# Kernel optimization log

Hardware: AMD Instinct MI355X
Metric: run time of the kernel (lower is better)

The kernel has to match this reference:

```python
import jax, jax.numpy as jnp
import numpy as np

HEADS = 2

def gat_layer(x, edge_index, W, att, bias):
    # x: [N, Fin], W: [H*C, Fin], att: [1, H, 2C], bias: [C]
    N = x.shape[0]
    C = bias.shape[0]
    # add self loops (source_to_target: x_j from row 0, aggregate onto row 1)
    loop = jnp.arange(N, dtype=edge_index.dtype)
    src = jnp.concatenate([edge_index[0], loop])
    dst = jnp.concatenate([edge_index[1], loop])
    h = (x @ W.T).reshape(N, HEADS, C)          # [N, H, C]
    x_j = h[src]                                 # [E, H, C]
    x_i = h[dst]                                 # [E, H, C]
    x_cat = jnp.concatenate([x_i, x_j], axis=-1) # [E, H, 2C]
    alpha = (x_cat * att).sum(-1)                # [E, H]
    alpha = jnp.where(alpha >= 0, alpha, 0.2 * alpha)  # leaky_relu(0.2)
    # NOTE: module uses a global (not per-destination) normalization
    alpha = jnp.exp(alpha - alpha.max())
    alpha = alpha / (alpha.sum(axis=0, keepdims=True) + 1e-10)
    msg = x_j * alpha[..., None]                 # [E, H, C]
    aggr = jax.ops.segment_sum(msg, dst, num_segments=N)  # [N, H, C]
    return aggr.mean(axis=1) + bias              # [N, C]

def setup_inputs() -> dict:
    key = jax.random.key(0)
    ks = jax.random.split(key, 7)
    N, Fin, C = 50000, 128, 64
    E = 800000
    x = jax.random.normal(ks[0], (N, Fin), dtype=jnp.float32)
    edge_index = jax.random.randint(ks[1], (2, E), 0, N, dtype=jnp.int64)
    W1 = jax.random.normal(ks[2], (HEADS * C, Fin), dtype=jnp.float32) * 0.05
    att1 = jax.random.normal(ks[3], (1, HEADS, 2 * C), dtype=jnp.float32) * 0.05
    b1 = jnp.zeros((C,), dtype=jnp.float32)
    W2 = jax.random.normal(ks[4], (HEADS * C, C), dtype=jnp.float32) * 0.05
    att2 = jax.random.normal(ks[5], (1, HEADS, 2 * C), dtype=jnp.float32) * 0.05
    b2 = jnp.zeros((C,), dtype=jnp.float32)
    return {"x": x, "edge_index": edge_index, "W1": W1, "att1": att1,
            "b1": b1, "W2": W2, "att2": att2, "b2": b2}

def reference(x, edge_index, W1, att1, b1, W2, att2, b2):
    h = gat_layer(x, edge_index, W1, att1, b1)
    h = jax.nn.relu(h)
    # F.dropout with training flag: treated as eval (identity) for determinism
    out = gat_layer(h, edge_index, W2, att2, b2)
    return out
```

## Files before the change

### kernel.cpp

```cpp
#include <hip/hip_runtime.h>
#include <hip/hip_bf16.h>
#include <math.h>


#define HP 8
#define HG 64
#define NHISTB (HP * HG)
#define HRANGE_MAX 6272
#define NSELF 16
#define NWGT  256

using short8 = __attribute__((ext_vector_type(8))) short;
using f32x4  = __attribute__((ext_vector_type(4))) float;

__device__ __forceinline__ unsigned f2bf(float x) {
  unsigned u = __float_as_uint(x);
  return (u + 0x7fffu + ((u >> 16) & 1u)) >> 16;
}
__device__ __forceinline__ float bflo(unsigned p) { return __uint_as_float(p << 16); }
__device__ __forceinline__ float bfhi(unsigned p) { return __uint_as_float(p & 0xffff0000u); }
__device__ __forceinline__ float lrexp(float a) {
  a = a >= 0.f ? a : 0.2f * a;
  return __expf(a);
}

__device__ __forceinline__ void block_zadd(float z0, float z1,
                                           float* __restrict__ Zp) {
  __shared__ float r0[16], r1[16];
  int lane = threadIdx.x & 63, w = threadIdx.x >> 6;
  int nw = blockDim.x >> 6;
#pragma unroll
  for (int off = 32; off; off >>= 1) {
    z0 += __shfl_down(z0, off, 64);
    z1 += __shfl_down(z1, off, 64);
  }
  if (lane == 0) { r0[w] = z0; r1[w] = z1; }
  __syncthreads();
  if (threadIdx.x == 0) {
    float s0 = 0.f, s1 = 0.f;
    for (int i = 0; i < nw; ++i) { s0 += r0[i]; s1 += r1[i]; }
    atomicAdd(&Zp[0], s0);
    atomicAdd(&Zp[1], s1);
  }
}

__global__ __launch_bounds__(256) void init_ws(
    const float* __restrict__ W1, const float* __restrict__ W2,
    unsigned short* __restrict__ wbf1, unsigned short* __restrict__ wbf2,
    float* __restrict__ Z, int* __restrict__ flags) {
  int tid = blockIdx.x * 256 + threadIdx.x;
  int stride = gridDim.x * 256;
  for (int i = tid; i < 128 * 128; i += stride)
    wbf1[i] = (unsigned short)f2bf(W1[i]);
  for (int i = tid; i < 128 * 64; i += stride)
    wbf2[i] = (unsigned short)f2bf(W2[i]);
  if (tid < 4) Z[tid] = 0.f;
  if (tid < 64) flags[tid] = -1;
}

template <int FIN, bool AB16>
__global__ __launch_bounds__(256) void gemm_mfma(
    const void* __restrict__ xin, const unsigned short* __restrict__ Wb,
    const float* __restrict__ att, unsigned* __restrict__ hq,
    float* __restrict__ si, float* __restrict__ sj,
    int N,
    const int* __restrict__ dstE, unsigned short* __restrict__ partial,
    int E, int nhistb, int hstep, int eper) {
  const int tid = threadIdx.x;

  constexpr int WB = 128 * FIN * 2;
  constexpr int SMEM = (WB > HRANGE_MAX * 4) ? WB : HRANGE_MAX * 4;
  __shared__ __align__(16) unsigned char smem[SMEM];

  if ((int)blockIdx.x < nhistb) {
    int* lhist = (int*)smem;
    const int p = blockIdx.x & (HP - 1);
    const int g = blockIdx.x >> 3;
    const int lo = p * hstep;
    for (int i = tid; i < hstep; i += 256) lhist[i] = 0;
    __syncthreads();
    const int eb = g * eper;
    const int ee = min(E, eb + eper);
    int e = eb + tid;
    for (; e + 3 * 256 < ee; e += 4 * 256) {
      int d0 = dstE[e] - lo;
      int d1 = dstE[e + 256] - lo;
      int d2 = dstE[e + 2 * 256] - lo;
      int d3 = dstE[e + 3 * 256] - lo;
      if ((unsigned)d0 < (unsigned)hstep) atomicAdd(&lhist[d0], 1);
      if ((unsigned)d1 < (unsigned)hstep) atomicAdd(&lhist[d1], 1);
      if ((unsigned)d2 < (unsigned)hstep) atomicAdd(&lhist[d2], 1);
      if ((unsigned)d3 < (unsigned)hstep) atomicAdd(&lhist[d3], 1);
    }
    for (; e < ee; e += 256) {
      int d = dstE[e] - lo;
      if ((unsigned)d < (unsigned)hstep) atomicAdd(&lhist[d], 1);
    }
    __syncthreads();
    for (int i = tid; i < hstep; i += 256) {
      int node = lo + i;
      if (node < N) partial[(size_t)g * N + node] = (unsigned short)lhist[i];
    }
    return;
  }

  constexpr int KS = FIN / 32;
  constexpr int CPR = FIN / 8;
  constexpr int NCHUNK = 128 * CPR;

  unsigned short* wlds = (unsigned short*)smem;

  const int w    = tid >> 6;
  const int lane = tid & 63;
  const int cl   = lane & 15;
  const int grp  = lane >> 4;
  const int n0   = (blockIdx.x - nhistb) * 64;

  const int arow = n0 + w * 16 + cl;
  const bool avalid = arow < N;

  short8 afrag[KS];
#pragma unroll
  for (int ks = 0; ks < KS; ++ks) {
    if constexpr (AB16) {
      short8 z = {0, 0, 0, 0, 0, 0, 0, 0};
      afrag[ks] = z;
      if (avalid) {
        const unsigned short* xb = (const unsigned short*)xin;
        afrag[ks] =
            *(const short8*)(xb + (size_t)arow * FIN + ks * 32 + grp * 8);
      }
    } else {
      float4 v0 = make_float4(0.f, 0.f, 0.f, 0.f), v1 = v0;
      if (avalid) {
        const float* xf = (const float*)xin;
        const float4* xp =
            (const float4*)(xf + (size_t)arow * FIN + ks * 32 + grp * 8);
        v0 = xp[0];
        v1 = xp[1];
      }
      union { short8 s8; unsigned u[4]; } af;
      af.u[0] = f2bf(v0.x) | (f2bf(v0.y) << 16);
      af.u[1] = f2bf(v0.z) | (f2bf(v0.w) << 16);
      af.u[2] = f2bf(v1.x) | (f2bf(v1.y) << 16);
      af.u[3] = f2bf(v1.z) | (f2bf(v1.w) << 16);
      afrag[ks] = af.s8;
    }
  }

  const uint4* Wb4 = (const uint4*)Wb;
  for (int c = tid; c < NCHUNK; c += 256) {
    int row = c / CPR;
    int cc  = c & (CPR - 1);
    *(uint4*)&wlds[row * FIN + ((cc ^ (row & (CPR - 1))) * 8)] = Wb4[c];
  }
  __syncthreads();

  f32x4 acc[8];
#pragma unroll
  for (int ct = 0; ct < 8; ++ct) acc[ct] = (f32x4){0.f, 0.f, 0.f, 0.f};

  const int swz = cl & (CPR - 1);
#pragma unroll
  for (int ks = 0; ks < KS; ++ks) {
#pragma unroll
    for (int ct = 0; ct < 8; ++ct) {
      const unsigned short* bp =
          &wlds[(ct * 16 + cl) * FIN + (((ks * 4 + grp) ^ swz) * 8)];
      short8 bfrag = *(const short8*)bp;
      acc[ct] = __builtin_amdgcn_mfma_f32_16x16x32_bf16(afrag[ks], bfrag,
                                                        acc[ct], 0, 0, 0);
    }
  }

  float ai[8], aj[8];
#pragma unroll
  for (int ct = 0; ct < 8; ++ct) {
    int hd = ct >> 2;
    int cw = (ct & 3) * 16 + cl;
    ai[ct] = att[hd * 128 + cw];
    aj[ct] = att[hd * 128 + 64 + cw];
  }

#pragma unroll
  for (int r = 0; r < 4; ++r) {
    int node = n0 + w * 16 + grp * 4 + r;
    float s0i = 0.f, s0j = 0.f, s1i = 0.f, s1j = 0.f;
    unsigned wpk[4];
#pragma unroll
    for (int ct = 0; ct < 4; ++ct) {
      float v0 = acc[ct][r];
      float v1 = acc[ct + 4][r];
      s0i += v0 * ai[ct];
      s0j += v0 * aj[ct];
      s1i += v1 * ai[ct + 4];
      s1j += v1 * aj[ct + 4];
      wpk[ct] = f2bf(v0) | (f2bf(v1) << 16);
    }
#pragma unroll
    for (int off = 8; off; off >>= 1) {
      s0i += __shfl_xor(s0i, off, 64);
      s0j += __shfl_xor(s0j, off, 64);
      s1i += __shfl_xor(s1i, off, 64);
      s1j += __shfl_xor(s1j, off, 64);
    }
    if (node < N) {
#pragma unroll
      for (int ct = 0; ct < 4; ++ct)
        hq[(size_t)node * 64 + ct * 16 + cl] = wpk[ct];
      if (cl == 0) {
        si[node * 2 + 0] = s0i;
        si[node * 2 + 1] = s1i;
        sj[node * 2 + 0] = s0j;
        sj[node * 2 + 1] = s1j;
      }
    }
  }
}

__global__ __launch_bounds__(256) void scan_full(
    unsigned short* __restrict__ partial, int* __restrict__ rowptr,
    int* __restrict__ flags, int N, int Eall, int nb) {
  __shared__ int ts[256];
  __shared__ int pre_s;
  const int b = blockIdx.x, t = threadIdx.x;
  const int base = b * 1024 + t * 4;
  int r0 = 0, r1 = 0, r2 = 0, r3 = 0;
  if (base < N) {
#pragma unroll 8
    for (int g = 0; g < HG; ++g) {
      unsigned long long* p =
          (unsigned long long*)&partial[(size_t)g * N + base];
      unsigned long long v = *p;
      *p = (unsigned long long)(unsigned short)r0 |
           ((unsigned long long)(unsigned short)r1 << 16) |
           ((unsigned long long)(unsigned short)r2 << 32) |
           ((unsigned long long)(unsigned short)r3 << 48);
      r0 += (int)(v & 0xffffu);
      r1 += (int)((v >> 16) & 0xffffu);
      r2 += (int)((v >> 32) & 0xffffu);
      r3 += (int)((v >> 48) & 0xffffu);
    }
  }
  const int tot = r0 + r1 + r2 + r3;
  ts[t] = tot;
  __syncthreads();
#pragma unroll
  for (int off = 1; off < 256; off <<= 1) {
    int x = (t >= off) ? ts[t - off] : 0;
    __syncthreads();
    ts[t] += x;
    __syncthreads();
  }
  const int run_local = ts[t] - tot;
  const int blktot = ts[255];
  if (t == 0)
    __hip_atomic_store(&flags[b], blktot, __ATOMIC_RELEASE,
                       __HIP_MEMORY_SCOPE_AGENT);
  __syncthreads();
  if (t < b) {
    int v;
    do {
      v = __hip_atomic_load(&flags[t], __ATOMIC_ACQUIRE,
                            __HIP_MEMORY_SCOPE_AGENT);
    } while (v < 0);
    ts[t] = v;
  }
  __syncthreads();
  if (t == 0) {
    int acc = 0;
    for (int i = 0; i < b; ++i) acc += ts[i];
    pre_s = acc;
  }
  __syncthreads();
  int run = pre_s + run_local;
  if (base < N) {
    rowptr[base] = run;         run += r0;
    rowptr[base + 1] = run;     run += r1;
    rowptr[base + 2] = run;     run += r2;
    rowptr[base + 3] = run;
  }
  if (b == nb - 1 && t == 255) rowptr[N] = Eall;
}

__global__ __launch_bounds__(1024) void scatter_z(
    const int* __restrict__ srcE, const int* __restrict__ dstE,
    const unsigned short* __restrict__ partial, const int* __restrict__ rowptr,
    float4* __restrict__ erec,
    const float2* __restrict__ si2, const float2* __restrict__ sj2,
    float* __restrict__ Zp, int E, int hstep, int N, int eper) {
  __shared__ __align__(16) int lcur[HRANGE_MAX];
  const int tid = threadIdx.x;
  float z0 = 0.f, z1 = 0.f;

  if ((int)blockIdx.x < NSELF) {
    for (int n = blockIdx.x * 1024 + tid; n < N; n += NSELF * 1024) {
      float2 a = si2[n], b = sj2[n];
      z0 += lrexp(a.x + b.x);
      z1 += lrexp(a.y + b.y);
    }
    block_zadd(z0, z1, Zp);
    return;
  }

  const int bid = blockIdx.x - NSELF;
  const int p = bid & (HP - 1);
  const int g = bid >> 3;
  const int lo = p * hstep;
  for (int i = tid; i < hstep; i += 1024) {
    int node = lo + i;
    lcur[i] = (node < N)
                  ? rowptr[node] + (int)partial[(size_t)g * N + node]
                  : 0;
  }
  __syncthreads();

  const int eb = g * eper;
  const int ee = min(E, eb + eper);
  int e = eb + tid;
  for (; e + 3 * 1024 < ee; e += 4 * 1024) {
    int d0 = dstE[e], d1 = dstE[e + 1024];
    int d2 = dstE[e + 2 * 1024], d3 = dstE[e + 3 * 1024];
    int s0 = srcE[e], s1 = srcE[e + 1024];
    int s2 = srcE[e + 2 * 1024], s3 = srcE[e + 3 * 1024];
    int t0 = d0 - lo, t1 = d1 - lo, t2 = d2 - lo, t3 = d3 - lo;
    if ((unsigned)t0 < (unsigned)hstep) {
      float2 siv = si2[d0], sjv = sj2[s0];
      float w0 = lrexp(siv.x + sjv.x), w1 = lrexp(siv.y + sjv.y);
      z0 += w0; z1 += w1;
      erec[atomicAdd(&lcur[t0], 1)] =
          make_float4(__int_as_float(s0), __int_as_float(d0), w0, w1);
    }
    if ((unsigned)t1 < (unsigned)hstep) {
      float2 siv = si2[d1], sjv = sj2[s1];
      float w0 = lrexp(siv.x + sjv.x), w1 = lrexp(siv.y + sjv.y);
      z0 += w0; z1 += w1;
      erec[atomicAdd(&lcur[t1], 1)] =
          make_float4(__int_as_float(s1), __int_as_float(d1), w0, w1);
    }
    if ((unsigned)t2 < (unsigned)hstep) {
      float2 siv = si2[d2], sjv = sj2[s2];
      float w0 = lrexp(siv.x + sjv.x), w1 = lrexp(siv.y + sjv.y);
      z0 += w0; z1 += w1;
      erec[atomicAdd(&lcur[t2], 1)] =
          make_float4(__int_as_float(s2), __int_as_float(d2), w0, w1);
    }
    if ((unsigned)t3 < (unsigned)hstep) {
      float2 siv = si2[d3], sjv = sj2[s3];
      float w0 = lrexp(siv.x + sjv.x), w1 = lrexp(siv.y + sjv.y);
      z0 += w0; z1 += w1;
      erec[atomicAdd(&lcur[t3], 1)] =
          make_float4(__int_as_float(s3), __int_as_float(d3), w0, w1);
    }
  }
  for (; e < ee; e += 1024) {
    int d = dstE[e];
    int dd = d - lo;
    if ((unsigned)dd < (unsigned)hstep) {
      int s = srcE[e];
      float2 siv = si2[d], sjv = sj2[s];
      float w0 = lrexp(siv.x + sjv.x), w1 = lrexp(siv.y + sjv.y);
      z0 += w0; z1 += w1;
      erec[atomicAdd(&lcur[dd], 1)] =
          make_float4(__int_as_float(s), __int_as_float(d), w0, w1);
    }
  }
  block_zadd(z0, z1, Zp);
}

__global__ __launch_bounds__(1024) void z_wgt2(
    const float2* __restrict__ si2, const float2* __restrict__ sj2,
    float* __restrict__ Zp, float4* __restrict__ erec, int E, int N) {
  const int tid = threadIdx.x;
  float z0 = 0.f, z1 = 0.f;
  if ((int)blockIdx.x < NSELF) {
    for (int n = blockIdx.x * 1024 + tid; n < N; n += NSELF * 1024) {
      float2 a = si2[n], b = sj2[n];
      z0 += lrexp(a.x + b.x);
      z1 += lrexp(a.y + b.y);
    }
  } else {
    int k = (blockIdx.x - NSELF) * 1024 + tid;
    for (; k < E; k += NWGT * 1024) {
      float4 r = erec[k];
      int s = __float_as_int(r.x);
      int d = __float_as_int(r.y);
      float2 siv = si2[d];
      float2 sjv = sj2[s];
      r.z = lrexp(siv.x + sjv.x);
      r.w = lrexp(siv.y + sjv.y);
      z0 += r.z; z1 += r.w;
      erec[k] = r;
    }
  }
  block_zadd(z0, z1, Zp);
}

__device__ __forceinline__ void edge8r(
    const float4* __restrict__ erec, int k, const unsigned* __restrict__ hq,
    int lane, float& acc0, float& acc1) {
  float4 r0 = erec[k],     r1 = erec[k + 1], r2 = erec[k + 2], r3 = erec[k + 3];
  float4 r4 = erec[k + 4], r5 = erec[k + 5], r6 = erec[k + 6], r7 = erec[k + 7];
  unsigned p0 = hq[(size_t)__float_as_int(r0.x) * 64 + lane];
  unsigned p1 = hq[(size_t)__float_as_int(r1.x) * 64 + lane];
  unsigned p2 = hq[(size_t)__float_as_int(r2.x) * 64 + lane];
  unsigned p3 = hq[(size_t)__float_as_int(r3.x) * 64 + lane];
  unsigned p4 = hq[(size_t)__float_as_int(r4.x) * 64 + lane];
  unsigned p5 = hq[(size_t)__float_as_int(r5.x) * 64 + lane];
  unsigned p6 = hq[(size_t)__float_as_int(r6.x) * 64 + lane];
  unsigned p7 = hq[(size_t)__float_as_int(r7.x) * 64 + lane];
  acc0 = fmaf(bflo(p0), r0.z, acc0);  acc1 = fmaf(bfhi(p0), r0.w, acc1);
  acc0 = fmaf(bflo(p1), r1.z, acc0);  acc1 = fmaf(bfhi(p1), r1.w, acc1);
  acc0 = fmaf(bflo(p2), r2.z, acc0);  acc1 = fmaf(bfhi(p2), r2.w, acc1);
  acc0 = fmaf(bflo(p3), r3.z, acc0);  acc1 = fmaf(bfhi(p3), r3.w, acc1);
  acc0 = fmaf(bflo(p4), r4.z, acc0);  acc1 = fmaf(bfhi(p4), r4.w, acc1);
  acc0 = fmaf(bflo(p5), r5.z, acc0);  acc1 = fmaf(bfhi(p5), r5.w, acc1);
  acc0 = fmaf(bflo(p6), r6.z, acc0);  acc1 = fmaf(bfhi(p6), r6.w, acc1);
  acc0 = fmaf(bflo(p7), r7.z, acc0);  acc1 = fmaf(bfhi(p7), r7.w, acc1);
}
__device__ __forceinline__ void edge4r(
    const float4* __restrict__ erec, int k, const unsigned* __restrict__ hq,
    int lane, float& acc0, float& acc1) {
  float4 r0 = erec[k], r1 = erec[k + 1], r2 = erec[k + 2], r3 = erec[k + 3];
  unsigned p0 = hq[(size_t)__float_as_int(r0.x) * 64 + lane];
  unsigned p1 = hq[(size_t)__float_as_int(r1.x) * 64 + lane];
  unsigned p2 = hq[(size_t)__float_as_int(r2.x) * 64 + lane];
  unsigned p3 = hq[(size_t)__float_as_int(r3.x) * 64 + lane];
  acc0 = fmaf(bflo(p0), r0.z, acc0);  acc1 = fmaf(bfhi(p0), r0.w, acc1);
  acc0 = fmaf(bflo(p1), r1.z, acc0);  acc1 = fmaf(bfhi(p1), r1.w, acc1);
  acc0 = fmaf(bflo(p2), r2.z, acc0);  acc1 = fmaf(bfhi(p2), r2.w, acc1);
  acc0 = fmaf(bflo(p3), r3.z, acc0);  acc1 = fmaf(bfhi(p3), r3.w, acc1);
}
__device__ __forceinline__ void edge1r(
    int s, float w0, float w1, const unsigned* __restrict__ hq, int lane,
    float& acc0, float& acc1) {
  unsigned p = hq[(size_t)s * 64 + lane];
  acc0 = fmaf(bflo(p), w0, acc0);
  acc1 = fmaf(bfhi(p), w1, acc1);
}

__global__ __launch_bounds__(256) void csr_aggregate(
    const int* __restrict__ rowptr, const float4* __restrict__ erec,
    const unsigned* __restrict__ hq, const float2* __restrict__ si2,
    const float2* __restrict__ sj2, const float* __restrict__ Zp,
    const float* __restrict__ bias, void* __restrict__ out,
    int N, int do_relu, int bf16_out) {
  int lane = threadIdx.x & 63;
  int wid = (blockIdx.x * blockDim.x + threadIdx.x) >> 6;
  int nw = (gridDim.x * blockDim.x) >> 6;
  float z0 = 1.f / (Zp[0] + 1e-10f);
  float z1 = 1.f / (Zp[1] + 1e-10f);
  float bv = bias[lane];
  for (int n0 = wid; n0 < N; n0 += nw) {
    int n = __builtin_amdgcn_readfirstlane(n0);
    int beg = rowptr[n], end = rowptr[n + 1];
    float2 siv = si2[n];
    float2 jv = sj2[n];
    float acc0 = 0.f, acc1 = 0.f;
    edge1r(n, lrexp(siv.x + jv.x), lrexp(siv.y + jv.y), hq, lane, acc0, acc1);
    int k = beg;
    for (; k + 8 <= end; k += 8) edge8r(erec, k, hq, lane, acc0, acc1);
    if (k + 4 <= end) { edge4r(erec, k, hq, lane, acc0, acc1); k += 4; }
    for (; k < end; ++k) {
      float4 r = erec[k];
      edge1r(__float_as_int(r.x), r.z, r.w, hq, lane, acc0, acc1);
    }
    float r = 0.5f * (acc0 * z0 + acc1 * z1) + bv;
    if (do_relu) r = fmaxf(r, 0.f);
    if (bf16_out)
      ((unsigned short*)out)[(size_t)n * 64 + lane] = (unsigned short)f2bf(r);
    else
      ((float*)out)[(size_t)n * 64 + lane] = r;
  }
}

extern "C" void kernel_launch(void* const* d_in, const int* in_sizes, int n_in,
                              void* d_out, int out_size, void* d_ws, size_t ws_size,
                              hipStream_t stream) {
  const float* x    = (const float*)d_in[0];
  const int*   ei   = (const int*)d_in[1];
  const float* W1   = (const float*)d_in[2];
  const float* att1 = (const float*)d_in[3];
  const float* b1   = (const float*)d_in[4];
  const float* W2   = (const float*)d_in[5];
  const float* att2 = (const float*)d_in[6];
  const float* b2   = (const float*)d_in[7];
  float* out = (float*)d_out;

  const int N = in_sizes[0] / 128;
  const int E = in_sizes[1] / 2;
  const int* srcE = ei;
  const int* dstE = ei + E;

  unsigned* hq = (unsigned*)d_ws;
  float* si    = (float*)(hq + (size_t)N * 64);
  float* sj    = si + (size_t)N * 2;
  float* Z     = sj + (size_t)N * 2;
  float* x2    = Z + 4;
  unsigned short* partial = (unsigned short*)x2;
  unsigned short* x2b = (unsigned short*)x2;
  int* rowptr  = (int*)(x2 + (size_t)N * 64);
  int* flags   = rowptr + (N + 1);
  uintptr_t ep = ((uintptr_t)(flags + 64) + 15) & ~(uintptr_t)15;
  float4* erec = (float4*)ep;
  unsigned short* wbf1 = (unsigned short*)(erec + E);
  unsigned short* wbf2 = wbf1 + 128 * 128;

  dim3 blk(256);
  dim3 blk1k(1024);
  int nb = (N + 1023) / 1024;
  int ntiles = (N + 63) / 64;
  int hstep = (N + HP - 1) / HP;
  int eper  = (E + HG - 1) / HG;

  init_ws<<<64, blk, 0, stream>>>(W1, W2, wbf1, wbf2, Z, flags);
  gemm_mfma<128, false><<<NHISTB + ntiles, blk, 0, stream>>>(
      x, wbf1, att1, hq, si, sj, N, dstE, partial, E, NHISTB, hstep, eper);
  scan_full<<<nb, blk, 0, stream>>>(partial, rowptr, flags, N, E, nb);
  scatter_z<<<NSELF + NHISTB, blk1k, 0, stream>>>(
      srcE, dstE, partial, rowptr, erec, (const float2*)si,
      (const float2*)sj, Z, E, hstep, N, eper);
  csr_aggregate<<<4096, blk, 0, stream>>>(rowptr, erec, hq,
                                          (const float2*)si, (const float2*)sj,
                                          Z, b1, x2b, N, 1, 1);
  gemm_mfma<64, true><<<ntiles, blk, 0, stream>>>(
      x2b, wbf2, att2, hq, si, sj, N, dstE, partial, E, 0, hstep, eper);
  z_wgt2<<<NSELF + NWGT, blk1k, 0, stream>>>(
      (const float2*)si, (const float2*)sj, Z + 2, erec, E, N);
  csr_aggregate<<<4096, blk, 0, stream>>>(rowptr, erec, hq,
                                          (const float2*)si, (const float2*)sj,
                                          Z + 2, b2, out, N, 0, 0);
}
```

Measured before the change: 238.0 us.

## Shrink edge records to 8 bytes with bf16 weights and CSR-walk layer-2 weights

The per-edge record drops from a 16-byte float4 (src, dst, w0, w1) to an 8-byte uint2 holding the source index and both attention weights packed as bf16. The layer-2 weight/Z kernel now walks the CSR row by row, one wave per destination, so the destination index no longer has to be stored and si2 is read once per row. This halves erec traffic in scatter, weight recompute and both aggregations, at the cost of bf16 precision on the attention weights. Z is still summed from the full fp32 weights.

Result: slower. 329.3 us (+38.4%).

```diff
diff --git a/kernel.cpp b/kernel.cpp
--- a/kernel.cpp
+++ b/kernel.cpp
@@ -8,7 +8,6 @@
 #define NHISTB (HP * HG)
 #define HRANGE_MAX 6272
 #define NSELF 16
-#define NWGT  256
 
 using short8 = __attribute__((ext_vector_type(8))) short;
 using f32x4  = __attribute__((ext_vector_type(4))) float;
@@ -286,7 +285,7 @@
 __global__ __launch_bounds__(1024) void scatter_z(
     const int* __restrict__ srcE, const int* __restrict__ dstE,
     const unsigned short* __restrict__ partial, const int* __restrict__ rowptr,
-    float4* __restrict__ erec,
+    uint2* __restrict__ erec,
     const float2* __restrict__ si2, const float2* __restrict__ sj2,
     float* __restrict__ Zp, int E, int hstep, int N, int eper) {
   __shared__ __align__(16) int lcur[HRANGE_MAX];
@@ -329,28 +328,28 @@
       float w0 = lrexp(siv.x + sjv.x), w1 = lrexp(siv.y + sjv.y);
       z0 += w0; z1 += w1;
       erec[atomicAdd(&lcur[t0], 1)] =
-          make_float4(__int_as_float(s0), __int_as_float(d0), w0, w1);
+          make_uint2((unsigned)s0, f2bf(w0) | (f2bf(w1) << 16));
     }
     if ((unsigned)t1 < (unsigned)hstep) {
       float2 siv = si2[d1], sjv = sj2[s1];
       float w0 = lrexp(siv.x + sjv.x), w1 = lrexp(siv.y + sjv.y);
       z0 += w0; z1 += w1;
       erec[atomicAdd(&lcur[t1], 1)] =
-          make_float4(__int_as_float(s1), __int_as_float(d1), w0, w1);
+          make_uint2((unsigned)s1, f2bf(w0) | (f2bf(w1) << 16));
     }
     if ((unsigned)t2 < (unsigned)hstep) {
       float2 siv = si2[d2], sjv = sj2[s2];
       float w0 = lrexp(siv.x + sjv.x), w1 = lrexp(siv.y + sjv.y);
       z0 += w0; z1 += w1;
       erec[atomicAdd(&lcur[t2], 1)] =
-          make_float4(__int_as_float(s2), __int_as_float(d2), w0, w1);
+          make_uint2((unsigned)s2, f2bf(w0) | (f2bf(w1) << 16));
     }
     if ((unsigned)t3 < (unsigned)hstep) {
       float2 siv = si2[d3], sjv = sj2[s3];
       float w0 = lrexp(siv.x + sjv.x), w1 = lrexp(siv.y + sjv.y);
       z0 += w0; z1 += w1;
       erec[atomicAdd(&lcur[t3], 1)] =
-          make_float4(__int_as_float(s3), __int_as_float(d3), w0, w1);
+          make_uint2((unsigned)s3, f2bf(w0) | (f2bf(w1) << 16));
     }
   }
   for (; e < ee; e += 1024) {
@@ -362,34 +361,36 @@
       float w0 = lrexp(siv.x + sjv.x), w1 = lrexp(siv.y + sjv.y);
       z0 += w0; z1 += w1;
       erec[atomicAdd(&lcur[dd], 1)] =
-          make_float4(__int_as_float(s), __int_as_float(d), w0, w1);
+          make_uint2((unsigned)s, f2bf(w0) | (f2bf(w1) << 16));
     }
   }
   block_zadd(z0, z1, Zp);
 }
 
-__global__ __launch_bounds__(1024) void z_wgt2(
+__global__ __launch_bounds__(256) void wgt2_z2(
+    const int* __restrict__ rowptr, uint2* __restrict__ erec,
     const float2* __restrict__ si2, const float2* __restrict__ sj2,
-    float* __restrict__ Zp, float4* __restrict__ erec, int E, int N) {
-  const int tid = threadIdx.x;
+    float* __restrict__ Zp, int N) {
+  int lane = threadIdx.x & 63;
+  int wid = (blockIdx.x * blockDim.x + threadIdx.x) >> 6;
+  int nw = (gridDim.x * blockDim.x) >> 6;
   float z0 = 0.f, z1 = 0.f;
-  if ((int)blockIdx.x < NSELF) {
-    for (int n = blockIdx.x * 1024 + tid; n < N; n += NSELF * 1024) {
-      float2 a = si2[n], b = sj2[n];
-      z0 += lrexp(a.x + b.x);
-      z1 += lrexp(a.y + b.y);
-    }
-  } else {
-    int k = (blockIdx.x - NSELF) * 1024 + tid;
-    for (; k < E; k += NWGT * 1024) {
-      float4 r = erec[k];
-      int s = __float_as_int(r.x);
-      int d = __float_as_int(r.y);
-      float2 siv = si2[d];
-      float2 sjv = sj2[s];
-      r.z = lrexp(siv.x + sjv.x);
-      r.w = lrexp(siv.y + sjv.y);
-      z0 += r.z; z1 += r.w;
+  for (int n0 = wid; n0 < N; n0 += nw) {
+    int n = __builtin_amdgcn_readfirstlane(n0);
+    int beg = rowptr[n], end = rowptr[n + 1];
+    float2 siv = si2[n];
+    if (lane == 0) {
+      float2 jv = sj2[n];
+      z0 += lrexp(siv.x + jv.x);
+      z1 += lrexp(siv.y + jv.y);
+    }
+    for (int k = beg + lane; k < end; k += 64) {
+      uint2 r = erec[k];
+      float2 jv = sj2[(int)r.x];
+      float w0 = lrexp(siv.x + jv.x);
+      float w1 = lrexp(siv.y + jv.y);
+      z0 += w0; z1 += w1;
+      r.y = f2bf(w0) | (f2bf(w1) << 16);
       erec[k] = r;
     }
   }
@@ -397,39 +398,39 @@
 }
 
 __device__ __forceinline__ void edge8r(
-    const float4* __restrict__ erec, int k, const unsigned* __restrict__ hq,
+    const uint2* __restrict__ erec, int k, const unsigned* __restrict__ hq,
     int lane, float& acc0, float& acc1) {
-  float4 r0 = erec[k],     r1 = erec[k + 1], r2 = erec[k + 2], r3 = erec[k + 3];
-  float4 r4 = erec[k + 4], r5 = erec[k + 5], r6 = erec[k + 6], r7 = erec[k + 7];
-  unsigned p0 = hq[(size_t)__float_as_int(r0.x) * 64 + lane];
-  unsigned p1 = hq[(size_t)__float_as_int(r1.x) * 64 + lane];
-  unsigned p2 = hq[(size_t)__float_as_int(r2.x) * 64 + lane];
-  unsigned p3 = hq[(size_t)__float_as_int(r3.x) * 64 + lane];
-  unsigned p4 = hq[(size_t)__float_as_int(r4.x) * 64 + lane];
-  unsigned p5 = hq[(size_t)__float_as_int(r5.x) * 64 + lane];
-  unsigned p6 = hq[(size_t)__float_as_int(r6.x) * 64 + lane];
-  unsigned p7 = hq[(size_t)__float_as_int(r7.x) * 64 + lane];
-  acc0 = fmaf(bflo(p0), r0.z, acc0);  acc1 = fmaf(bfhi(p0), r0.w, acc1);
-  acc0 = fmaf(bflo(p1), r1.z, acc0);  acc1 = fmaf(bfhi(p1), r1.w, acc1);
-  acc0 = fmaf(bflo(p2), r2.z, acc0);  acc1 = fmaf(bfhi(p2), r2.w, acc1);
-  acc0 = fmaf(bflo(p3), r3.z, acc0);  acc1 = fmaf(bfhi(p3), r3.w, acc1);
-  acc0 = fmaf(bflo(p4), r4.z, acc0);  acc1 = fmaf(bfhi(p4), r4.w, acc1);
-  acc0 = fmaf(bflo(p5), r5.z, acc0);  acc1 = fmaf(bfhi(p5), r5.w, acc1);
-  acc0 = fmaf(bflo(p6), r6.z, acc0);  acc1 = fmaf(bfhi(p6), r6.w, acc1);
-  acc0 = fmaf(bflo(p7), r7.z, acc0);  acc1 = fmaf(bfhi(p7), r7.w, acc1);
+  uint2 r0 = erec[k],     r1 = erec[k + 1], r2 = erec[k + 2], r3 = erec[k + 3];
+  uint2 r4 = erec[k + 4], r5 = erec[k + 5], r6 = erec[k + 6], r7 = erec[k + 7];
+  unsigned p0 = hq[(size_t)r0.x * 64 + lane];
+  unsigned p1 = hq[(size_t)r1.x * 64 + lane];
+  unsigned p2 = hq[(size_t)r2.x * 64 + lane];
+  unsigned p3 = hq[(size_t)r3.x * 64 + lane];
+  unsigned p4 = hq[(size_t)r4.x * 64 + lane];
+  unsigned p5 = hq[(size_t)r5.x * 64 + lane];
+  unsigned p6 = hq[(size_t)r6.x * 64 + lane];
+  unsigned p7 = hq[(size_t)r7.x * 64 + lane];
+  acc0 = fmaf(bflo(p0), bflo(r0.y), acc0);  acc1 = fmaf(bfhi(p0), bfhi(r0.y), acc1);
+  acc0 = fmaf(bflo(p1), bflo(r1.y), acc0);  acc1 = fmaf(bfhi(p1), bfhi(r1.y), acc1);
+  acc0 = fmaf(bflo(p2), bflo(r2.y), acc0);  acc1 = fmaf(bfhi(p2), bfhi(r2.y), acc1);
+  acc0 = fmaf(bflo(p3), bflo(r3.y), acc0);  acc1 = fmaf(bfhi(p3), bfhi(r3.y), acc1);
+  acc0 = fmaf(bflo(p4), bflo(r4.y), acc0);  acc1 = fmaf(bfhi(p4), bfhi(r4.y), acc1);
+  acc0 = fmaf(bflo(p5), bflo(r5.y), acc0);  acc1 = fmaf(bfhi(p5), bfhi(r5.y), acc1);
+  acc0 = fmaf(bflo(p6), bflo(r6.y), acc0);  acc1 = fmaf(bfhi(p6), bfhi(r6.y), acc1);
+  acc0 = fmaf(bflo(p7), bflo(r7.y), acc0);  acc1 = fmaf(bfhi(p7), bfhi(r7.y), acc1);
 }
 __device__ __forceinline__ void edge4r(
-    const float4* __restrict__ erec, int k, const unsigned* __restrict__ hq,
+    const uint2* __restrict__ erec, int k, const unsigned* __restrict__ hq,
     int lane, float& acc0, float& acc1) {
-  float4 r0 = erec[k], r1 = erec[k + 1], r2 = erec[k + 2], r3 = erec[k + 3];
-  unsigned p0 = hq[(size_t)__float_as_int(r0.x) * 64 + lane];
-  unsigned p1 = hq[(size_t)__float_as_int(r1.x) * 64 + lane];
-  unsigned p2 = hq[(size_t)__float_as_int(r2.x) * 64 + lane];
-  unsigned p3 = hq[(size_t)__float_as_int(r3.x) * 64 + lane];
-  acc0 = fmaf(bflo(p0), r0.z, acc0);  acc1 = fmaf(bfhi(p0), r0.w, acc1);
-  acc0 = fmaf(bflo(p1), r1.z, acc0);  acc1 = fmaf(bfhi(p1), r1.w, acc1);
-  acc0 = fmaf(bflo(p2), r2.z, acc0);  acc1 = fmaf(bfhi(p2), r2.w, acc1);
-  acc0 = fmaf(bflo(p3), r3.z, acc0);  acc1 = fmaf(bfhi(p3), r3.w, acc1);
+  uint2 r0 = erec[k], r1 = erec[k + 1], r2 = erec[k + 2], r3 = erec[k + 3];
+  unsigned p0 = hq[(size_t)r0.x * 64 + lane];
+  unsigned p1 = hq[(size_t)r1.x * 64 + lane];
+  unsigned p2 = hq[(size_t)r2.x * 64 + lane];
+  unsigned p3 = hq[(size_t)r3.x * 64 + lane];
+  acc0 = fmaf(bflo(p0), bflo(r0.y), acc0);  acc1 = fmaf(bfhi(p0), bfhi(r0.y), acc1);
+  acc0 = fmaf(bflo(p1), bflo(r1.y), acc0);  acc1 = fmaf(bfhi(p1), bfhi(r1.y), acc1);
+  acc0 = fmaf(bflo(p2), bflo(r2.y), acc0);  acc1 = fmaf(bfhi(p2), bfhi(r2.y), acc1);
+  acc0 = fmaf(bflo(p3), bflo(r3.y), acc0);  acc1 = fmaf(bfhi(p3), bfhi(r3.y), acc1);
 }
 __device__ __forceinline__ void edge1r(
     int s, float w0, float w1, const unsigned* __restrict__ hq, int lane,
@@ -440,7 +441,7 @@
 }
 
 __global__ __launch_bounds__(256) void csr_aggregate(
-    const int* __restrict__ rowptr, const float4* __restrict__ erec,
+    const int* __restrict__ rowptr, const uint2* __restrict__ erec,
     const unsigned* __restrict__ hq, const float2* __restrict__ si2,
     const float2* __restrict__ sj2, const float* __restrict__ Zp,
     const float* __restrict__ bias, void* __restrict__ out,
@@ -462,8 +463,8 @@
     for (; k + 8 <= end; k += 8) edge8r(erec, k, hq, lane, acc0, acc1);
     if (k + 4 <= end) { edge4r(erec, k, hq, lane, acc0, acc1); k += 4; }
     for (; k < end; ++k) {
-      float4 r = erec[k];
-      edge1r(__float_as_int(r.x), r.z, r.w, hq, lane, acc0, acc1);
+      uint2 r = erec[k];
+      edge1r((int)r.x, bflo(r.y), bfhi(r.y), hq, lane, acc0, acc1);
     }
     float r = 0.5f * (acc0 * z0 + acc1 * z1) + bv;
     if (do_relu) r = fmaxf(r, 0.f);
@@ -502,7 +503,7 @@
   int* rowptr  = (int*)(x2 + (size_t)N * 64);
   int* flags   = rowptr + (N + 1);
   uintptr_t ep = ((uintptr_t)(flags + 64) + 15) & ~(uintptr_t)15;
-  float4* erec = (float4*)ep;
+  uint2* erec  = (uint2*)ep;
   unsigned short* wbf1 = (unsigned short*)(erec + E);
   unsigned short* wbf2 = wbf1 + 128 * 128;
 
@@ -525,8 +526,8 @@
                                           Z, b1, x2b, N, 1, 1);
   gemm_mfma<64, true><<<ntiles, blk, 0, stream>>>(
       x2b, wbf2, att2, hq, si, sj, N, dstE, partial, E, 0, hstep, eper);
-  z_wgt2<<<NSELF + NWGT, blk1k, 0, stream>>>(
-      (const float2*)si, (const float2*)sj, Z + 2, erec, E, N);
+  wgt2_z2<<<4096, blk, 0, stream>>>(rowptr, erec, (const float2*)si,
+                                    (const float2*)sj, Z + 2, N);
   csr_aggregate<<<4096, blk, 0, stream>>>(rowptr, erec, hq,
                                           (const float2*)si, (const float2*)sj,
                                           Z + 2, b2, out, N, 0, 0);
```
